# Kernel tuning notes

Measured on AMD Instinct MI355X. Metric: run time of the kernel, lower is better.

The kernel has to match this reference:

```python
import jax, jax.numpy as jnp
import numpy as np

WS = 11      # window_size
C = 3        # channels
SIGMA = 1.5
C1 = 0.01 ** 2
C2 = 0.03 ** 2


def _gaussian_window():
    # 1D gaussian, normalized, then outer product -> [C, 1, WS, WS] depthwise kernel
    x = jnp.arange(WS, dtype=jnp.float32)
    g = jnp.exp(-((x - WS // 2) ** 2) / (2.0 * SIGMA ** 2))
    g = g / g.sum()
    w2d = jnp.outer(g, g)  # [WS, WS]
    return jnp.broadcast_to(w2d[None, None], (C, 1, WS, WS))


def _dwconv(x, w):
    # depthwise conv2d, SAME padding (pad = WS//2, odd kernel)
    pad = WS // 2
    return jax.lax.conv_general_dilated(
        x, w, window_strides=(1, 1), padding=[(pad, pad), (pad, pad)],
        dimension_numbers=("NCHW", "OIHW", "NCHW"), feature_group_count=C)


def setup_inputs() -> dict:
    key = jax.random.key(0)
    k1, k2 = jax.random.split(key)
    pred = jax.random.uniform(k1, (16, 3, 512, 512), dtype=jnp.float32)
    target = jax.random.uniform(k2, (16, 3, 512, 512), dtype=jnp.float32)
    return {"pred": pred, "target": target}


def reference(pred, target):
    w = _gaussian_window()
    mu1 = _dwconv(pred, w)
    mu2 = _dwconv(target, w)
    mu1_sq = mu1 * mu1
    mu2_sq = mu2 * mu2
    mu1_mu2 = mu1 * mu2
    sigma1_sq = _dwconv(pred * pred, w) - mu1_sq
    sigma2_sq = _dwconv(target * target, w) - mu2_sq
    sigma12 = _dwconv(pred * target, w) - mu1_mu2
    ssim_map = ((2.0 * mu1_mu2 + C1) * (2.0 * sigma12 + C2)) / (
        (mu1_sq + mu2_sq + C1) * (sigma1_sq + sigma2_sq + C2))
    return 1.0 - ssim_map.mean()
```

## Files before the change

kernel.cpp:

```cpp
#include <hip/hip_runtime.h>


#define IMG 512
#define NCHAN 48
#define TW 32
#define TH 64
#define HR (TH + 10)
#define PST 33

constexpr double RW1 = 0.8007374029168082;
constexpr double RW2 = 0.4111122905071876;
constexpr double RW3 = 0.1353352832366127;
constexpr double RW4 = 0.0285655007845504;
constexpr double RW5 = 0.0038659201394728;
constexpr double RSUM = 1.0 + 2.0 * (RW1 + RW2 + RW3 + RW4 + RW5);
constexpr float GW[11] = {
    (float)(RW5 / RSUM), (float)(RW4 / RSUM), (float)(RW3 / RSUM),
    (float)(RW2 / RSUM), (float)(RW1 / RSUM), (float)(1.0 / RSUM),
    (float)(RW1 / RSUM), (float)(RW2 / RSUM), (float)(RW3 / RSUM),
    (float)(RW4 / RSUM), (float)(RW5 / RSUM)};

__device__ __forceinline__ float2 pk_scale(float w, float2 a) {
  return make_float2(w * a.x, w * a.y);
}
__device__ __forceinline__ float2 pk_add(float2 a, float2 b) {
  return make_float2(a.x + b.x, a.y + b.y);
}
__device__ __forceinline__ float2 pk_fma2(float2 a, float2 b, float2 c) {
  return make_float2(fmaf(a.x, b.x, c.x), fmaf(a.y, b.y, c.y));
}

template <bool CHECKED>
__device__ __forceinline__ void hload(const float* __restrict__ P,
                                      const float* __restrict__ T, int r0t,
                                      int c0, int j, float4* vp, float4* vt) {
  const int g = j & 7;
  const int h = j >> 3;
  const int gy = r0t - 5 + h;
  const int gx0 = c0 + g * 4 - 8;
  if (CHECKED) {
    const bool rowok = (gy >= 0) && (gy < IMG);
    const float* __restrict__ Prow = P + (size_t)gy * IMG;
    const float* __restrict__ Trow = T + (size_t)gy * IMG;
#pragma unroll
    for (int q = 0; q < 5; ++q) {
      const int gx = gx0 + q * 4;
      vp[q] = make_float4(0.f, 0.f, 0.f, 0.f);
      vt[q] = vp[q];
      if (rowok && gx >= 0 && gx < IMG) {
        vp[q] = *(const float4*)(Prow + gx);
        vt[q] = *(const float4*)(Trow + gx);
      }
    }
  } else {
    const float* __restrict__ Prow = P + (size_t)gy * IMG + gx0;
    const float* __restrict__ Trow = T + (size_t)gy * IMG + gx0;
#pragma unroll
    for (int q = 0; q < 5; ++q) {
      vp[q] = *(const float4*)(Prow + q * 4);
      vt[q] = *(const float4*)(Trow + q * 4);
    }
  }
}

__device__ __forceinline__ void hcompute(int j, const float4* vp,
                                         const float4* vt,
                                         float4 (*hs)[PST]) {
  const int g = j & 7;
  const int h = j >> 3;
  float2 uv[20];
#pragma unroll
  for (int q = 0; q < 5; ++q) {
    const float4 p4 = vp[q], t4 = vt[q];
    uv[q * 4 + 0] = make_float2(p4.x + t4.x, p4.x - t4.x);
    uv[q * 4 + 1] = make_float2(p4.y + t4.y, p4.y - t4.y);
    uv[q * 4 + 2] = make_float2(p4.z + t4.z, p4.z - t4.z);
    uv[q * 4 + 3] = make_float2(p4.w + t4.w, p4.w - t4.w);
  }
#pragma unroll
  for (int o = 0; o < 4; ++o) {
    float2 amu = make_float2(0.f, 0.f);
    float2 asq = make_float2(0.f, 0.f);
#pragma unroll
    for (int k = 0; k < 11; ++k) {
      const float2 e = uv[3 + o + k];
      const float2 t1 = pk_scale(GW[k], e);
      amu = pk_add(amu, t1);
      asq = pk_fma2(t1, e, asq);
    }
    hs[h][g * 4 + o] = make_float4(amu.x, amu.y, asq.x, asq.y);
  }
}

template <bool CHECKED>
__device__ __forceinline__ void phase_b(const float* __restrict__ P,
                                        const float* __restrict__ T, int r0t,
                                        int c0, int tid, float4 (*hs)[PST]) {
  float4 ap[5], at[5], bp[5], bt[5];
  hload<CHECKED>(P, T, r0t, c0, tid, ap, at);
  hload<CHECKED>(P, T, r0t, c0, tid + 256, bp, bt);
  hcompute(tid, ap, at, hs);
  hcompute(tid + 256, bp, bt, hs);
  if (tid < HR * 8 - 512) {
    hload<CHECKED>(P, T, r0t, c0, tid + 512, ap, at);
    hcompute(tid + 512, ap, at, hs);
  }
}

__global__ __launch_bounds__(256, 4) void ssim_main(
    const float* __restrict__ pred, const float* __restrict__ tgt,
    double* __restrict__ ws) {
  __shared__ float4 hs[HR][PST];
  __shared__ float wsum[4];

  const int tid = threadIdx.x;
  const int c0 = blockIdx.x * TW;
  const int r0t = blockIdx.y * TH;
  const int nc = blockIdx.z;
  const size_t base = (size_t)nc * IMG * IMG;
  const float* __restrict__ P = pred + base;
  const float* __restrict__ T = tgt + base;

  const bool interior =
      (c0 != 0) && (c0 != IMG - TW) && (r0t != 0) && (r0t != IMG - TH);
  if (interior)
    phase_b<false>(P, T, r0t, c0, tid, hs);
  else
    phase_b<true>(P, T, r0t, c0, tid, hs);
  __syncthreads();

  float lsum = 0.f;
  {
    const int x = tid & (TW - 1);
    const int r0 = (tid >> 5) * 8;
    float2 amu[8], asq[8];
#pragma unroll
    for (int o = 0; o < 8; ++o) {
      amu[o] = make_float2(0.f, 0.f);
      asq[o] = make_float2(0.f, 0.f);
    }
#pragma unroll
    for (int j = 0; j < 18; ++j) {
      const float4 h4 = hs[r0 + j][x];
      const float2 hmu = make_float2(h4.x, h4.y);
      const float2 hsq = make_float2(h4.z, h4.w);
#pragma unroll
      for (int o = 0; o < 8; ++o) {
        const int k = j - o;
        if (k >= 0 && k < 11) {
          const float w = GW[k];
          amu[o] = pk_fma2(make_float2(w, w), hmu, amu[o]);
          asq[o] = pk_fma2(make_float2(w, w), hsq, asq[o]);
        }
      }
    }
#pragma unroll
    for (int o = 0; o < 8; ++o) {
      const float cu = amu[o].x, cv = amu[o].y;
      const float cu2 = asq[o].x, cv2 = asq[o].y;
      const float cusq = cu * cu, cvsq = cv * cv;
      const float mu12 = 0.25f * (cusq - cvsq);
      const float musq = 0.5f * (cusq + cvsq);
      const float s12 = 0.25f * (cu2 - cv2);
      const float ssq = 0.5f * (cu2 + cv2);
      const float num = (2.f * mu12 + 1e-4f) * (2.f * (s12 - mu12) + 9e-4f);
      const float den = (musq + 1e-4f) * (ssq - musq + 9e-4f);
      lsum += num * __builtin_amdgcn_rcpf(den);
    }
  }

#pragma unroll
  for (int off = 32; off > 0; off >>= 1) lsum += __shfl_down(lsum, off, 64);
  if ((tid & 63) == 0) wsum[tid >> 6] = lsum;
  __syncthreads();
  if (tid == 0) {
    const float bsum = wsum[0] + wsum[1] + wsum[2] + wsum[3];
    unsafeAtomicAdd(&ws[nc], (double)bsum);
  }
}

__global__ void ssim_fin(const double* __restrict__ ws,
                         float* __restrict__ out) {
  const int l = threadIdx.x;
  double v = (l < NCHAN) ? ws[l] : 0.0;
#pragma unroll
  for (int off = 32; off > 0; off >>= 1) v += __shfl_down(v, off, 64);
  if (l == 0) out[0] = (float)(1.0 - v / (double)(IMG * IMG * NCHAN));
}

extern "C" void kernel_launch(void* const* d_in, const int* in_sizes, int n_in,
                              void* d_out, int out_size, void* d_ws,
                              size_t ws_size, hipStream_t stream) {
  const float* pred = (const float*)d_in[0];
  const float* tgt = (const float*)d_in[1];
  double* ws = (double*)d_ws;

  hipMemsetAsync(d_ws, 0, NCHAN * sizeof(double), stream);
  dim3 grid(IMG / TW, IMG / TH, NCHAN);
  ssim_main<<<grid, 256, 0, stream>>>(pred, tgt, ws);
  ssim_fin<<<1, 64, 0, stream>>>(ws, (float*)d_out);
}
```

Baseline: 158.1 us.

## Store horizontal-pass intermediates as packed bf16 in LDS and raise occupancy

The horizontal blur results (sum/difference means and second moments) are rounded to bf16 and packed two per 32-bit word, so the shared tile shrinks from float4 to uint2 per pixel. The smaller LDS footprint and the launch bound raised from 4 to 8 blocks per CU are meant to allow more resident blocks and halve LDS traffic. The cost is extra conversion ALU work and bf16 rounding of the variance terms, which can introduce noticeable error in sigma, since it is computed as the difference of two similar quantities. Explicit packed float2 math is also replaced with scalar fmas.

```diff
diff --git a/kernel.cpp b/kernel.cpp
--- a/kernel.cpp
+++ b/kernel.cpp
@@ -20,14 +20,18 @@
     (float)(RW1 / RSUM), (float)(RW2 / RSUM), (float)(RW3 / RSUM),
     (float)(RW4 / RSUM), (float)(RW5 / RSUM)};
 
-__device__ __forceinline__ float2 pk_scale(float w, float2 a) {
-  return make_float2(w * a.x, w * a.y);
-}
-__device__ __forceinline__ float2 pk_add(float2 a, float2 b) {
-  return make_float2(a.x + b.x, a.y + b.y);
-}
-__device__ __forceinline__ float2 pk_fma2(float2 a, float2 b, float2 c) {
-  return make_float2(fmaf(a.x, b.x, c.x), fmaf(a.y, b.y, c.y));
+__device__ __forceinline__ unsigned bf16_rne(float x) {
+  const unsigned u = __float_as_uint(x);
+  return (u + 0x7fffu + ((u >> 16) & 1u)) >> 16;
+}
+__device__ __forceinline__ unsigned pk_bf16(float a, float b) {
+  return bf16_rne(a) | (bf16_rne(b) << 16);
+}
+__device__ __forceinline__ float bf_lo(unsigned u) {
+  return __uint_as_float(u << 16);
+}
+__device__ __forceinline__ float bf_hi(unsigned u) {
+  return __uint_as_float(u & 0xffff0000u);
 }
 
 template <bool CHECKED>
@@ -64,8 +68,7 @@
 }
 
 __device__ __forceinline__ void hcompute(int j, const float4* vp,
-                                         const float4* vt,
-                                         float4 (*hs)[PST]) {
+                                         const float4* vt, uint2 (*hs)[PST]) {
   const int g = j & 7;
   const int h = j >> 3;
   float2 uv[20];
@@ -77,25 +80,33 @@
     uv[q * 4 + 2] = make_float2(p4.z + t4.z, p4.z - t4.z);
     uv[q * 4 + 3] = make_float2(p4.w + t4.w, p4.w - t4.w);
   }
+  uint2 outp[4];
 #pragma unroll
   for (int o = 0; o < 4; ++o) {
-    float2 amu = make_float2(0.f, 0.f);
-    float2 asq = make_float2(0.f, 0.f);
+    float cu = 0.f, cv = 0.f, cu2 = 0.f, cv2 = 0.f;
 #pragma unroll
     for (int k = 0; k < 11; ++k) {
       const float2 e = uv[3 + o + k];
-      const float2 t1 = pk_scale(GW[k], e);
-      amu = pk_add(amu, t1);
-      asq = pk_fma2(t1, e, asq);
-    }
-    hs[h][g * 4 + o] = make_float4(amu.x, amu.y, asq.x, asq.y);
-  }
+      const float wu = GW[k] * e.x;
+      const float wv = GW[k] * e.y;
+      cu += wu;
+      cv += wv;
+      cu2 = fmaf(wu, e.x, cu2);
+      cv2 = fmaf(wv, e.y, cv2);
+    }
+    outp[o].x = pk_bf16(cu, cv);
+    outp[o].y = pk_bf16(cu2, cv2);
+  }
+  *(uint4*)&hs[h][g * 4] = make_uint4(outp[0].x, outp[0].y, outp[1].x,
+                                      outp[1].y);
+  *(uint4*)&hs[h][g * 4 + 2] = make_uint4(outp[2].x, outp[2].y, outp[3].x,
+                                          outp[3].y);
 }
 
 template <bool CHECKED>
 __device__ __forceinline__ void phase_b(const float* __restrict__ P,
                                         const float* __restrict__ T, int r0t,
-                                        int c0, int tid, float4 (*hs)[PST]) {
+                                        int c0, int tid, uint2 (*hs)[PST]) {
   float4 ap[5], at[5], bp[5], bt[5];
   hload<CHECKED>(P, T, r0t, c0, tid, ap, at);
   hload<CHECKED>(P, T, r0t, c0, tid + 256, bp, bt);
@@ -107,10 +118,10 @@
   }
 }
 
-__global__ __launch_bounds__(256, 4) void ssim_main(
+__global__ __launch_bounds__(256, 8) void ssim_main(
     const float* __restrict__ pred, const float* __restrict__ tgt,
     double* __restrict__ ws) {
-  __shared__ float4 hs[HR][PST];
+  __shared__ uint2 hs[HR][PST];
   __shared__ float wsum[4];
 
   const int tid = threadIdx.x;
@@ -141,16 +152,18 @@
     }
 #pragma unroll
     for (int j = 0; j < 18; ++j) {
-      const float4 h4 = hs[r0 + j][x];
-      const float2 hmu = make_float2(h4.x, h4.y);
-      const float2 hsq = make_float2(h4.z, h4.w);
+      const uint2 hv = hs[r0 + j][x];
+      const float hcu = bf_lo(hv.x), hcv = bf_hi(hv.x);
+      const float hc2u = bf_lo(hv.y), hc2v = bf_hi(hv.y);
 #pragma unroll
       for (int o = 0; o < 8; ++o) {
         const int k = j - o;
         if (k >= 0 && k < 11) {
           const float w = GW[k];
-          amu[o] = pk_fma2(make_float2(w, w), hmu, amu[o]);
-          asq[o] = pk_fma2(make_float2(w, w), hsq, asq[o]);
+          amu[o].x = fmaf(w, hcu, amu[o].x);
+          amu[o].y = fmaf(w, hcv, amu[o].y);
+          asq[o].x = fmaf(w, hc2u, asq[o].x);
+          asq[o].y = fmaf(w, hc2v, asq[o].y);
         }
       }
     }
@@ -195,7 +208,7 @@
   const float* tgt = (const float*)d_in[1];
   double* ws = (double*)d_ws;
 
-  hipMemsetAsync(d_ws, 0, NCHAN * sizeof(double), stream);
+  (void)hipMemsetAsync(d_ws, 0, NCHAN * sizeof(double), stream);
   dim3 grid(IMG / TW, IMG / TH, NCHAN);
   ssim_main<<<grid, 256, 0, stream>>>(pred, tgt, ws);
   ssim_fin<<<1, 64, 0, stream>>>(ws, (float*)d_out);
```

Result: slower. 219.4 us (+38.8%).
